# Optimization experiments

Hardware: AMD Instinct MI355X
Metric: run time of the kernel (lower is better)

The kernel has to match this reference:

```python
import jax, jax.numpy as jnp
import numpy as np

B, T, S, A = 4, 10, 6, 6
HID, L, IMG = 512, 6, 128
NCH = 16  # spatial-softmax channels
_px, _py = np.meshgrid(np.linspace(-1.0, 1.0, IMG), np.linspace(-1.0, 1.0, IMG))
POSX = jnp.asarray(_px.reshape(-1), jnp.float32)
POSY = jnp.asarray(_py.reshape(-1), jnp.float32)


def _conv_relu(x, w, b):
    y = jax.lax.conv_general_dilated(x, w, (1, 1), 'SAME',
                                     dimension_numbers=('NCHW', 'OIHW', 'NCHW'))
    return jax.nn.relu(y + b[None, :, None, None])


def _cnn_ss(x, ws, bs):
    for w, b in zip(ws, bs):
        x = _conv_relu(x, w, b)
    n = x.shape[0]
    attn = jax.nn.softmax(x.reshape(n, NCH, -1), axis=-1)  # (n, 16, H*W)
    ex = attn @ POSX  # (n, 16)
    ey = attn @ POSY
    return jnp.stack([ex, ey], axis=-1).reshape(n, 2 * NCH)  # (n, 32)


def _lstm_cell(x, h, c, wih, whh, bih, bhh):
    g = x @ wih.T + bih + h @ whh.T + bhh
    i, f, gg, o = jnp.split(g, 4, axis=-1)  # torch LSTMCell gate order i,f,g,o
    c2 = jax.nn.sigmoid(f) * c + jax.nn.sigmoid(i) * jnp.tanh(gg)
    h2 = jax.nn.sigmoid(o) * jnp.tanh(c2)
    return h2, c2


def setup_inputs() -> dict:
    key = jax.random.key(0)
    ks = iter(jax.random.split(key, 64))

    def nrm(shape, s=0.05):
        return jax.random.normal(next(ks), shape, dtype=jnp.float32) * s

    inp = {
        'seq_img_main': nrm((B, T, 3, IMG, IMG), 1.0),
        'seq_img_secondary': nrm((B, T, 3, IMG, IMG), 1.0),
        'seq_states': nrm((B, T, S), 1.0),
    }
    chans = [(32, 3), (64, 32), (128, 64), (16, 128)]
    for cam in ('m', 's'):
        for j, (o, ci) in enumerate(chans):
            inp[f'{cam}_w{j}'] = nrm((o, ci, 3, 3))
            inp[f'{cam}_b{j}'] = nrm((o,))
    in0, inr = S + 64, HID + 64  # 70 and 576
    inp['wih0'] = nrm((4 * HID, in0)); inp['whh0'] = nrm((4 * HID, HID))
    inp['bih0'] = nrm((4 * HID,)); inp['bhh0'] = nrm((4 * HID,))
    inp['wih_r'] = nrm((L - 1, 4 * HID, inr)); inp['whh_r'] = nrm((L - 1, 4 * HID, HID))
    inp['bih_r'] = nrm((L - 1, 4 * HID)); inp['bhh_r'] = nrm((L - 1, 4 * HID))
    inp['out_w'] = nrm((A, inr)); inp['out_b'] = nrm((A,))
    return inp


def reference(seq_img_main, seq_img_secondary, seq_states,
              m_w0, m_b0, m_w1, m_b1, m_w2, m_b2, m_w3, m_b3,
              s_w0, s_b0, s_w1, s_b1, s_w2, s_b2, s_w3, s_b3,
              wih0, whh0, bih0, bhh0, wih_r, whh_r, bih_r, bhh_r,
              out_w, out_b):
    b, t = seq_img_main.shape[:2]
    fm = _cnn_ss(seq_img_main.reshape(b * t, 3, IMG, IMG),
                 [m_w0, m_w1, m_w2, m_w3], [m_b0, m_b1, m_b2, m_b3])
    fs = _cnn_ss(seq_img_secondary.reshape(b * t, 3, IMG, IMG),
                 [s_w0, s_w1, s_w2, s_w3], [s_b0, s_b1, s_b2, s_b3])
    img = jnp.concatenate([fm, fs], axis=-1).reshape(b, t, 64)  # (B,T,64)

    h0 = jnp.zeros((L, b, HID), jnp.float32)
    c0 = jnp.zeros((L, b, HID), jnp.float32)

    def step(carry, xt):
        h, c = carry
        st, im = xt  # (B,S), (B,64)
        x = jnp.concatenate([st, im], axis=-1)
        hn, cn = _lstm_cell(x, h[0], c[0], wih0, whh0, bih0, bhh0)
        hs, cs = [hn], [cn]
        for l in range(L - 1):
            x = jnp.concatenate([hs[-1], im], axis=-1)
            hl, cl = _lstm_cell(x, h[l + 1], c[l + 1],
                                wih_r[l], whh_r[l], bih_r[l], bhh_r[l])
            hs.append(hl); cs.append(cl)
        out = jnp.concatenate([hs[-1], im], axis=-1) @ out_w.T + out_b
        return (jnp.stack(hs), jnp.stack(cs)), out

    _, outs = jax.lax.scan(step, (h0, c0),
                           (seq_states.transpose(1, 0, 2), img.transpose(1, 0, 2)))
    return outs.transpose(1, 0, 2)  # (B,T,A)
```

## Files before the change

### kernel.cpp

```cpp
#include <hip/hip_runtime.h>
#include <hip/hip_bf16.h>
#include <math.h>

typedef __hip_bfloat16 bf16;
typedef short bf16x8 __attribute__((ext_vector_type(8)));
typedef float f32x4 __attribute__((ext_vector_type(4)));

static constexpr int HWPX = 16384;
static constexpr int NBL  = 16;

__device__ inline float sigmoidf_(float x) { return 1.0f / (1.0f + expf(-x)); }
__device__ inline float bflo(unsigned u) { return __uint_as_float(u << 16); }
__device__ inline float bfhi(unsigned u) { return __uint_as_float(u & 0xffff0000u); }
__device__ inline int swz(int x) { return (x ^ (x >> 2)) & 3; }

__device__ inline void gll16(const bf16* g, short* l) {
    __builtin_amdgcn_global_load_lds(
        (const __attribute__((address_space(1))) void*)g,
        (__attribute__((address_space(3))) void*)l, 16, 0, 0);
}

__device__ inline int flag_ld(const int* p) {
    return __hip_atomic_load(p, __ATOMIC_RELAXED, __HIP_MEMORY_SCOPE_AGENT);
}
__device__ inline void flag_st(int* p, int v) {
    __hip_atomic_store(p, v, __ATOMIC_RELAXED, __HIP_MEMORY_SCOPE_AGENT);
}
__device__ inline unsigned long long devload2(const float* p) {
    return __hip_atomic_load((const unsigned long long*)p,
                             __ATOMIC_RELAXED, __HIP_MEMORY_SCOPE_AGENT);
}
__device__ inline void devstore(float* p, float v) {
    __hip_atomic_store(p, v, __ATOMIC_RELAXED, __HIP_MEMORY_SCOPE_AGENT);
}

__global__ __launch_bounds__(256) void prep_lstm_k(
    const float* __restrict__ wih0, const float* __restrict__ whh0,
    const float* __restrict__ wihr, const float* __restrict__ whhr,
    bf16* __restrict__ d0, bf16* __restrict__ d1,
    bf16* __restrict__ d2, bf16* __restrict__ d3)
{
    const size_t nA = 2048ull * 72, nB = 2048ull * 512;
    const size_t nC = 5ull * 2048 * 576, nD = 5ull * 2048 * 512;
    for (size_t i = blockIdx.x * 256ull + threadIdx.x; i < nA + nB + nC + nD;
         i += (size_t)gridDim.x * 256) {
        if (i < nA) {
            int c = (int)(i % 72), r = (int)(i / 72);
            d0[i] = __float2bfloat16(c < 70 ? wih0[(size_t)r * 70 + c] : 0.f);
        } else if (i < nA + nB) {
            size_t k = i - nA; d1[k] = __float2bfloat16(whh0[k]);
        } else if (i < nA + nB + nC) {
            size_t k = i - nA - nB; d2[k] = __float2bfloat16(wihr[k]);
        } else {
            size_t k = i - nA - nB - nC; d3[k] = __float2bfloat16(whhr[k]);
        }
    }
}

struct ConvW {
    const float* src[8];
    bf16* dst[8];
};

__global__ __launch_bounds__(256) void prep_conv_k(ConvW a)
{
    const int sizes[4] = {3072, 18432, 73728, 18432};
    const int cins[4] = {3, 32, 64, 128};
    const int couts[4] = {32, 64, 128, 16};
    int total = 2 * 113664;
    for (int idx = blockIdx.x * 256 + threadIdx.x; idx < total; idx += gridDim.x * 256) {
        int i = idx, cam = 0;
        if (i >= 113664) { cam = 1; i -= 113664; }
        int layer = 0;
        while (layer < 3 && i >= sizes[layer]) { i -= sizes[layer]; ++layer; }
        const float* w = a.src[cam * 4 + layer];
        bf16* d = a.dst[cam * 4 + layer];
        if (layer == 0) {
            int k = i & 31, co = (i >> 5) & 31, ky = i >> 10;
            int kx = k >> 3, c = k & 7;
            float v = (kx < 3 && c < 3) ? w[((co * 3 + c) * 3 + ky) * 3 + kx] : 0.f;
            d[i] = __float2bfloat16(v);
        } else {
            int CIN = cins[layer], COUT = couts[layer], KC = CIN / 32;
            int e = i & 7;
            int t2 = i >> 3;
            int co = t2 % COUT;
            int t3 = t2 / COUT;
            int q = t3 & 3;
            int t4 = t3 >> 2;
            int kc = t4 % KC;
            int tap = t4 / KC;
            d[i] = __float2bfloat16(w[((size_t)(co * CIN + kc * 32 + q * 8 + e)) * 9 + tap]);
        }
    }
}

__global__ __launch_bounds__(256) void conv0_nhwc(
    const float* __restrict__ srcm, const float* __restrict__ srcs,
    const bf16* __restrict__ w0m, const bf16* __restrict__ w0s,
    const float* __restrict__ bm, const float* __restrict__ bs,
    bf16* __restrict__ out, int c0)
{
    const int y = blockIdx.x;
    const int cam = blockIdx.y;
    const int img = blockIdx.z;
    const int ci_ = cam * gridDim.z + img;
    const float* inImg = (cam ? srcs : srcm) + (size_t)(c0 + img) * 3 * HWPX;
    const bf16* wT0 = cam ? w0s : w0m;
    const float* bias = cam ? bs : bm;
    const int tid = threadIdx.x;
    const int wave = tid >> 6, lane = tid & 63;
    const int wm = wave & 1, wn = wave >> 1;
    const int q = lane >> 4, n16 = lane & 15;

    __shared__ short smem[3 * 130 * 16];

    for (int d = tid; d < 3 * 130; d += 256) {
        int x = d % 130, r = d / 130;
        int yy = y + r - 1, xx = x - 1;
        bf16 v8[8];
#pragma unroll
        for (int c = 0; c < 8; ++c) v8[c] = __float2bfloat16(0.f);
        if ((unsigned)yy < 128u && (unsigned)xx < 128u) {
            int o = yy * 128 + xx;
            v8[0] = __float2bfloat16(inImg[o]);
            v8[1] = __float2bfloat16(inImg[HWPX + o]);
            v8[2] = __float2bfloat16(inImg[2 * HWPX + o]);
        }
        *(bf16x8*)(void*)&smem[(r * 130 + x) * 16] = *(bf16x8*)(void*)v8;
        *(bf16x8*)(void*)&smem[(r * 130 + x) * 16 + 8] = (bf16x8)0;
    }
    __syncthreads();

    f32x4 acc[4];
#pragma unroll
    for (int nt = 0; nt < 4; ++nt) acc[nt] = f32x4{0.f, 0.f, 0.f, 0.f};

    const int co = wm * 16 + n16;
#pragma unroll
    for (int ky = 0; ky < 3; ++ky) {
        bf16x8 aF = *(const bf16x8*)(const void*)(wT0 + ((size_t)(ky * 32 + co) * 32) + q * 8);
#pragma unroll
        for (int nt = 0; nt < 4; ++nt) {
            int x = (wn * 4 + nt) * 16 + n16;
            int off = (q < 3) ? (ky * 130 + x + q) * 16 : (ky * 130 + x) * 16 + 8;
            bf16x8 bF = *(const bf16x8*)(const void*)&smem[off];
            acc[nt] = __builtin_amdgcn_mfma_f32_16x16x32_bf16(aF, bF, acc[nt], 0, 0, 0);
        }
    }

    int co0 = wm * 16 + q * 4;
#pragma unroll
    for (int nt = 0; nt < 4; ++nt) {
        int x = (wn * 4 + nt) * 16 + n16;
        bf16 tmp[4];
#pragma unroll
        for (int r = 0; r < 4; ++r) {
            float v = acc[nt][r] + bias[co0 + r];
            tmp[r] = __float2bfloat16(v > 0.f ? v : 0.f);
        }
        *reinterpret_cast<uint2*>(out + ((size_t)ci_ * HWPX + y * 128 + x) * 32 + co0)
            = *reinterpret_cast<uint2*>(tmp);
    }
}

template <int CIN, int COUT>
__global__ __launch_bounds__(256, 4) void conv2r(
    const bf16* __restrict__ in, const bf16* __restrict__ wTm,
    const bf16* __restrict__ wTs, const float* __restrict__ bm,
    const float* __restrict__ bs, bf16* __restrict__ out,
    const char* __restrict__ zpage)
{
    constexpr int KC = CIN / 32;
    constexpr int NB = (KC > 1) ? 2 : 1;
    constexpr int MW = COUT / 32;
    constexpr int SLOTS = 4 * 264;

    const int y0 = (blockIdx.x >> 1) * 2;
    const int x0 = (blockIdx.x & 1) * 64;
    const int cam = blockIdx.y;
    const int img = blockIdx.z;
    const int ci_ = cam * gridDim.z + img;
    const bf16* wT = cam ? wTs : wTm;
    const float* bias = cam ? bs : bm;
    const int tid = threadIdx.x;
    const int wave = tid >> 6, lane = tid & 63;
    const int wrow = wave >> 1, wm = wave & 1;
    const int q = lane >> 4, n16 = lane & 15;

    __shared__ short smem[NB][SLOTS * 8];
    const bf16* inImg = in + (size_t)ci_ * HWPX * CIN;

    const bf16* sptr[5];
#pragma unroll
    for (int it = 0; it < 5; ++it) {
        int s = it * 256 + tid;
        int r = s / 264, s2 = s - r * 264;
        int sx = s2 >> 2;
        int g = (s2 & 3) ^ swz(sx);
        int yy = y0 + r - 1, xx = x0 + sx - 1;
        bool ok = (s < SLOTS) && ((unsigned)yy < 128u) && ((unsigned)xx < 128u);
        sptr[it] = ok ? inImg + ((size_t)yy * 128 + xx) * CIN + g * 8
                      : (const bf16*)(zpage + (tid & 255) * 16);
    }
    auto stage = [&](int kc, int buf) {
#pragma unroll
        for (int it = 0; it < 5; ++it) {
            if (it * 256 + tid < SLOTS)
                gll16(sptr[it] + kc * 32, &smem[buf][it * 2048 + wave * 512]);
        }
    };

    f32x4 acc[MW][4];
#pragma unroll
    for (int mt = 0; mt < MW; ++mt)
#pragma unroll
        for (int nt = 0; nt < 4; ++nt) acc[mt][nt] = f32x4{0.f, 0.f, 0.f, 0.f};

    stage(0, 0);
    for (int kc = 0; kc < KC; ++kc) {
        __syncthreads();
        if (kc + 1 < KC) stage(kc + 1, (kc + 1) % NB);
        const short* sb = smem[kc % NB];
#pragma unroll
        for (int ky = 0; ky < 3; ++ky) {
#pragma unroll
            for (int kx = 0; kx < 3; ++kx) {
                bf16x8 aF[MW];
#pragma unroll
                for (int mt = 0; mt < MW; ++mt) {
                    int co = (wm * MW + mt) * 16 + n16;
                    aF[mt] = *(const bf16x8*)(const void*)(wT +
                        ((((size_t)(ky * 3 + kx) * KC + kc) * 4 + q) * COUT + co) * 8);
                }
#pragma unroll
                for (int nt = 0; nt < 4; ++nt) {
                    int xt = nt * 16 + n16 + kx;
                    int slot = (wrow + ky) * 264 + xt * 4 + (q ^ swz(xt));
                    bf16x8 bF = *(const bf16x8*)(const void*)&sb[slot * 8];
#pragma unroll
                    for (int mt = 0; mt < MW; ++mt)
                        acc[mt][nt] = __builtin_amdgcn_mfma_f32_16x16x32_bf16(
                            aF[mt], bF, acc[mt][nt], 0, 0, 0);
                }
            }
        }
    }

    const int y = y0 + wrow;
#pragma unroll
    for (int mt = 0; mt < MW; ++mt) {
        int co0 = (wm * MW + mt) * 16 + q * 4;
#pragma unroll
        for (int nt = 0; nt < 4; ++nt) {
            int x = x0 + nt * 16 + n16;
            bf16 tmp[4];
#pragma unroll
            for (int r = 0; r < 4; ++r) {
                float v = acc[mt][nt][r] + bias[co0 + r];
                tmp[r] = __float2bfloat16(v > 0.f ? v : 0.f);
            }
            *reinterpret_cast<uint2*>(out + ((size_t)ci_ * HWPX + y * 128 + x) * COUT + co0)
                = *reinterpret_cast<uint2*>(tmp);
        }
    }
}

__global__ __launch_bounds__(256, 6) void conv4_xs(
    const bf16* __restrict__ in, const bf16* __restrict__ wTm,
    const bf16* __restrict__ wTs, const float* __restrict__ bm,
    const float* __restrict__ bs,
    float* __restrict__ partial,
    const char* __restrict__ zpage, int c0)
{
    constexpr int CIN = 128, COUT = 16, KC = 4;
    constexpr int SLOTS = 3 * 66 * 4;
    const int y = blockIdx.x >> 1;
    const int xh = blockIdx.x & 1;
    const int x0 = xh * 64;
    const int cam = blockIdx.y;
    const int img = blockIdx.z;
    const int ci_ = cam * gridDim.z + img;
    const int gimg = cam * 40 + c0 + img;
    const bf16* wT = cam ? wTs : wTm;
    const float* bias = cam ? bs : bm;
    const int tid = threadIdx.x;
    const int wave = tid >> 6, lane = tid & 63;
    const int q = lane >> 4, n16 = lane & 15;

    __shared__ short smem[2][SLOTS * 8];
    __shared__ float sred[3][4][16];
    const bf16* inImg = in + (size_t)ci_ * HWPX * CIN;

    const bf16* sptr[4];
#pragma unroll
    for (int it = 0; it < 4; ++it) {
        int s = it * 256 + tid;
        int r = s / 264, s2 = s - r * 264;
        int sx = s2 >> 2;
        int g = (s2 & 3) ^ swz(sx);
        int yy = y + r - 1, xx = x0 + sx - 1;
        bool ok = (s < SLOTS) && ((unsigned)yy < 128u) && ((unsigned)xx < 128u);
        sptr[it] = ok ? inImg + ((size_t)yy * 128 + xx) * CIN + g * 8
                      : (const bf16*)(zpage + (tid & 255) * 16);
    }
    auto stage = [&](int kc, int buf) {
#pragma unroll
        for (int it = 0; it < 4; ++it) {
            if (it * 256 + tid < SLOTS)
                gll16(sptr[it] + kc * 32, &smem[buf][it * 2048 + wave * 512]);
        }
    };

    f32x4 acc = f32x4{0.f, 0.f, 0.f, 0.f};

    stage(0, 0);
    for (int kc = 0; kc < KC; ++kc) {
        __syncthreads();
        if (kc + 1 < KC) stage(kc + 1, (kc + 1) & 1);
        const short* sb = smem[kc & 1];
#pragma unroll
        for (int ky = 0; ky < 3; ++ky) {
#pragma unroll
            for (int kx = 0; kx < 3; ++kx) {
                bf16x8 aF = *(const bf16x8*)(const void*)(wT +
                    ((((size_t)(ky * 3 + kx) * KC + kc) * 4 + q) * COUT + n16) * 8);
                int xt = wave * 16 + n16 + kx;
                int slot = xt * 4 + (q ^ swz(xt));
                bf16x8 bF = *(const bf16x8*)(const void*)&sb[ky * 2112 + slot * 8];
                acc = __builtin_amdgcn_mfma_f32_16x16x32_bf16(aF, bF, acc, 0, 0, 0);
            }
        }
    }

    float v[4];
    int x = x0 + wave * 16 + n16;
    float px = -1.f + (2.f / 127.f) * x;
#pragma unroll
    for (int r = 0; r < 4; ++r) {
        float t = acc[r] + bias[q * 4 + r];
        v[r] = t > 0.f ? t : 0.f;
    }
    float M[4];
#pragma unroll
    for (int r = 0; r < 4; ++r) {
        M[r] = v[r];
        M[r] = fmaxf(M[r], __shfl_xor(M[r], 1));
        M[r] = fmaxf(M[r], __shfl_xor(M[r], 2));
        M[r] = fmaxf(M[r], __shfl_xor(M[r], 4));
        M[r] = fmaxf(M[r], __shfl_xor(M[r], 8));
    }
    if (n16 == 0)
#pragma unroll
        for (int r = 0; r < 4; ++r) sred[0][wave][q * 4 + r] = M[r];
    __syncthreads();
#pragma unroll
    for (int r = 0; r < 4; ++r) {
        M[r] = fmaxf(fmaxf(sred[0][0][q * 4 + r], sred[0][1][q * 4 + r]),
                     fmaxf(sred[0][2][q * 4 + r], sred[0][3][q * 4 + r]));
    }
    float s[4], sx[4];
#pragma unroll
    for (int r = 0; r < 4; ++r) {
        float e = expf(v[r] - M[r]);
        s[r] = e; sx[r] = e * px;
        s[r] += __shfl_xor(s[r], 1);  sx[r] += __shfl_xor(sx[r], 1);
        s[r] += __shfl_xor(s[r], 2);  sx[r] += __shfl_xor(sx[r], 2);
        s[r] += __shfl_xor(s[r], 4);  sx[r] += __shfl_xor(sx[r], 4);
        s[r] += __shfl_xor(s[r], 8);  sx[r] += __shfl_xor(sx[r], 8);
    }
    __syncthreads();
    if (n16 == 0)
#pragma unroll
        for (int r = 0; r < 4; ++r) {
            sred[1][wave][q * 4 + r] = s[r];
            sred[2][wave][q * 4 + r] = sx[r];
        }
    __syncthreads();
    if (tid < 16) {
        float S = sred[1][0][tid] + sred[1][1][tid] + sred[1][2][tid] + sred[1][3][tid];
        float SX = sred[2][0][tid] + sred[2][1][tid] + sred[2][2][tid] + sred[2][3][tid];
        float Mv = fmaxf(fmaxf(sred[0][0][tid], sred[0][1][tid]),
                         fmaxf(sred[0][2][tid], sred[0][3][tid]));
        float* pp = partial + (((size_t)gimg * 16 + tid) * 256 + (y * 2 + xh)) * 4;
        pp[0] = Mv; pp[1] = S; pp[2] = SX;
    }
}

__global__ __launch_bounds__(256) void ssmerge_k(
    const float* __restrict__ partial, float* __restrict__ featm,
    float* __restrict__ feats)
{
    const int img = blockIdx.x;
    const int cam = img / 40, li = img % 40;
    float* feat = cam ? feats : featm;
    const int tid = threadIdx.x;
    const int co = tid >> 4, s = tid & 15;
    const float* base = partial + ((size_t)img * 16 + co) * 256 * 4;
    float M = -1e30f, S = 0.f, SX = 0.f, SY = 0.f;
    for (int i = s; i < 256; i += 16) {
        float m = base[i * 4], sv = base[i * 4 + 1], sxv = base[i * 4 + 2];
        float py = -1.f + (2.f / 127.f) * (i >> 1);
        float Mn = fmaxf(M, m);
        float w0 = expf(M - Mn), w1 = expf(m - Mn);
        S = S * w0 + sv * w1;
        SX = SX * w0 + sxv * w1;
        SY = SY * w0 + sv * py * w1;
        M = Mn;
    }
#pragma unroll
    for (int mask = 1; mask < 16; mask <<= 1) {
        float Mo = __shfl_xor(M, mask), So = __shfl_xor(S, mask);
        float SXo = __shfl_xor(SX, mask), SYo = __shfl_xor(SY, mask);
        float Mn = fmaxf(M, Mo);
        float w0 = expf(M - Mn), w1 = expf(Mo - Mn);
        S = S * w0 + So * w1; SX = SX * w0 + SXo * w1; SY = SY * w0 + SYo * w1;
        M = Mn;
    }
    if (s == 0) {
        feat[(size_t)li * 32 + 2 * co] = SX / S;
        feat[(size_t)li * 32 + 2 * co + 1] = SY / S;
    }
}

__device__ inline float imgfeat(const float* featm, const float* feats,
                                int b, int t, int k)
{
    int idx = (b * 10 + t) * 32;
    return k < 32 ? featm[idx + k] : feats[idx + k - 32];
}

template <int NB1>
__device__ inline void cell_mm(const bf16* __restrict__ wih,
                               const bf16* __restrict__ whh,
                               const float* __restrict__ xs0,
                               int j, int sub, float (&dg)[4][4])
{
    constexpr int K1 = NB1 * 8;
    constexpr int XS = K1 + 512;
#pragma unroll
    for (int r = 0; r < 4; ++r) {
        const uint4* __restrict__ w1 =
            reinterpret_cast<const uint4*>(wih + (size_t)(j + r * 512) * K1);
#pragma unroll
        for (int g0 = 0; g0 < NB1; g0 += 8) {
            int g = g0 + sub;
            if (g0 + 7 < NB1 || g < NB1) {
                uint4 u = w1[g];
                float a0 = bflo(u.x), a1 = bfhi(u.x), a2 = bflo(u.y), a3 = bfhi(u.y);
                float a4 = bflo(u.z), a5 = bfhi(u.z), a6 = bflo(u.w), a7 = bfhi(u.w);
#pragma unroll
                for (int b = 0; b < 4; ++b) {
                    const float* xp = xs0 + b * XS + g * 8;
                    dg[r][b] += a0 * xp[0] + a1 * xp[1] + a2 * xp[2] + a3 * xp[3]
                              + a4 * xp[4] + a5 * xp[5] + a6 * xp[6] + a7 * xp[7];
                }
            }
        }
        const uint4* __restrict__ w2 =
            reinterpret_cast<const uint4*>(whh + (size_t)(j + r * 512) * 512);
#pragma unroll
        for (int gi = 0; gi < 8; ++gi) {
            int g = gi * 8 + sub;
            uint4 u = w2[g];
            float a0 = bflo(u.x), a1 = bfhi(u.x), a2 = bflo(u.y), a3 = bfhi(u.y);
            float a4 = bflo(u.z), a5 = bfhi(u.z), a6 = bflo(u.w), a7 = bfhi(u.w);
#pragma unroll
            for (int b = 0; b < 4; ++b) {
                const float* xp = xs0 + b * XS + K1 + g * 8;
                dg[r][b] += a0 * xp[0] + a1 * xp[1] + a2 * xp[2] + a3 * xp[3]
                          + a4 * xp[4] + a5 * xp[5] + a6 * xp[6] + a7 * xp[7];
            }
        }
    }
}

template <int NB1>
__device__ inline void lstm_layer_loop(
    int l, int bx,
    const bf16* __restrict__ wih, const bf16* __restrict__ whh,
    const float* __restrict__ bih, const float* __restrict__ bhh,
    const float* __restrict__ states,
    const float* __restrict__ featm, const float* __restrict__ feats,
    float* __restrict__ hAll, float* __restrict__ cst,
    int* __restrict__ fl, float* __restrict__ xs)
{
    constexpr int K1 = NB1 * 8;
    constexpr int XS = K1 + 512;
    const int tid = threadIdx.x;
    const int jloc = tid >> 3;
    const int sub = tid & 7;
    const int j = bx * 32 + jloc;

    for (int t = 0; t < 10; ++t) {
        if (l > 0 && tid < 16) {
            while (flag_ld(&fl[(l - 1) * 16 + tid]) < t + 1)
                __builtin_amdgcn_s_sleep(1);
        }
        if (t > 0 && tid >= 64 && tid < 80) {
            while (flag_ld(&fl[l * 16 + (tid - 64)]) < t)
                __builtin_amdgcn_s_sleep(1);
        }
        __syncthreads();

        const float* hprev = (l == 0) ? nullptr
                           : hAll + ((size_t)(t + 1) * 6 + (l - 1)) * 2048;
        const float* hold  = hAll + ((size_t)t * 6 + l) * 2048;
        float* hnew        = hAll + ((size_t)(t + 1) * 6 + l) * 2048;

        if (NB1 == 72) {
            for (int i = tid; i < 4 * 512; i += 256) {
                int bb = i >> 9, kk = i & 511;
                union { unsigned long long u; float f[2]; } cv;
                int base;
                if (kk < 256) { cv.u = devload2(&hprev[bb * 512 + kk * 2]); base = bb * XS + kk * 2; }
                else { cv.u = devload2(&hold[bb * 512 + (kk - 256) * 2]); base = bb * XS + 576 + (kk - 256) * 2; }
                xs[base] = cv.f[0]; xs[base + 1] = cv.f[1];
            }
            {
                int bb = tid >> 6, k = tid & 63;
                xs[bb * XS + 512 + k] = imgfeat(featm, feats, bb, t, k);
            }
        } else {
            for (int i = tid; i < 4 * 256; i += 256) {
                int bb = i >> 8, kk = i & 255;
                union { unsigned long long u; float f[2]; } cv;
                cv.u = devload2(&hold[bb * 512 + kk * 2]);
                int base = bb * XS + 72 + kk * 2;
                xs[base] = cv.f[0]; xs[base + 1] = cv.f[1];
            }
            for (int i = tid; i < 4 * 72; i += 256) {
                int bb = i / 72, k = i - bb * 72;
                float v = (k < 6) ? states[(bb * 10 + t) * 6 + k]
                                  : (k < 70 ? imgfeat(featm, feats, bb, t, k - 6) : 0.f);
                xs[bb * XS + k] = v;
            }
        }
        __syncthreads();

        float dg[4][4] = {{0.f, 0.f, 0.f, 0.f}, {0.f, 0.f, 0.f, 0.f},
                          {0.f, 0.f, 0.f, 0.f}, {0.f, 0.f, 0.f, 0.f}};
        cell_mm<NB1>(wih, whh, xs, j, sub, dg);

#pragma unroll
        for (int r = 0; r < 4; ++r)
#pragma unroll
            for (int b = 0; b < 4; ++b) {
                dg[r][b] += __shfl_xor(dg[r][b], 1);
                dg[r][b] += __shfl_xor(dg[r][b], 2);
                dg[r][b] += __shfl_xor(dg[r][b], 4);
            }

        if (sub == 0) {
            float b0 = bih[j] + bhh[j];
            float b1 = bih[j + 512] + bhh[j + 512];
            float b2 = bih[j + 1024] + bhh[j + 1024];
            float b3 = bih[j + 1536] + bhh[j + 1536];
#pragma unroll
            for (int b = 0; b < 4; ++b) {
                float gi = dg[0][b] + b0;
                float gf = dg[1][b] + b1;
                float gg = dg[2][b] + b2;
                float go = dg[3][b] + b3;
                float cp = cst[b * 512 + j];
                float c2 = sigmoidf_(gf) * cp + sigmoidf_(gi) * tanhf(gg);
                float h2 = sigmoidf_(go) * tanhf(c2);
                cst[b * 512 + j] = c2;
                devstore(&hnew[b * 512 + j], h2);
            }
        }
        __syncthreads();
        if (tid == 0) flag_st(&fl[l * 16 + bx], t + 1);
    }
}

__global__ __launch_bounds__(256) void lstm_pipe_k(
    const bf16* __restrict__ wih0p, const bf16* __restrict__ whh0b,
    const bf16* __restrict__ wihrb, const bf16* __restrict__ whhrb,
    const float* __restrict__ bih0, const float* __restrict__ bhh0,
    const float* __restrict__ bihr, const float* __restrict__ bhhr,
    const float* __restrict__ states,
    const float* __restrict__ featm, const float* __restrict__ feats,
    float* __restrict__ hAll, float* __restrict__ cAll,
    const float* __restrict__ out_w, const float* __restrict__ out_b,
    float* __restrict__ out, int* __restrict__ fl)
{
    const int gb = blockIdx.x;
    const int tid = threadIdx.x;
    __shared__ float xs[4 * 1088];

    if (gb == 6 * NBL) {
        for (int t = 0; t < 10; ++t) {
            if (tid < 16) {
                while (flag_ld(&fl[5 * 16 + tid]) < t + 1)
                    __builtin_amdgcn_s_sleep(1);
            }
            __syncthreads();
            const float* h5 = hAll + ((size_t)(t + 1) * 6 + 5) * 2048;
            int p = tid >> 3, sub = tid & 7;
            if (p < 24) {
                int b = p / 6, a = p % 6;
                const float* wr = out_w + a * 576;
                float acc = 0.f;
                for (int k = sub; k < 256; k += 8) {
                    union { unsigned long long u; float f[2]; } cv;
                    cv.u = devload2(&h5[b * 512 + k * 2]);
                    acc += wr[k * 2] * cv.f[0] + wr[k * 2 + 1] * cv.f[1];
                }
                for (int k = sub; k < 64; k += 8)
                    acc += wr[512 + k] * imgfeat(featm, feats, b, t, k);
                acc += __shfl_xor(acc, 1);
                acc += __shfl_xor(acc, 2);
                acc += __shfl_xor(acc, 4);
                if (sub == 0) out[(b * 10 + t) * 6 + a] = acc + out_b[a];
            }
            __syncthreads();
        }
        return;
    }

    const int l = gb / NBL;
    const int bx = gb % NBL;

    const bf16 *wih, *whh;
    const float *bih, *bhh;
    if (l == 0) { wih = wih0p; whh = whh0b; bih = bih0; bhh = bhh0; }
    else {
        wih = wihrb + (size_t)(l - 1) * 2048 * 576;
        whh = whhrb + (size_t)(l - 1) * 2048 * 512;
        bih = bihr + (l - 1) * 2048;
        bhh = bhhr + (l - 1) * 2048;
    }
    float* cst = cAll + (size_t)l * 2048;

    if (l > 0) {
        const int jloc = tid >> 3, sub = tid & 7;
        const int j = bx * 32 + jloc;
        unsigned wsum = 0;
        for (int r = 0; r < 4; ++r) {
            const uint4* w1 = reinterpret_cast<const uint4*>(wih + (size_t)(j + r * 512) * 576);
            for (int g = sub; g < 72; g += 8) { uint4 u = w1[g]; wsum ^= u.x ^ u.w; }
            const uint4* w2 = reinterpret_cast<const uint4*>(whh + (size_t)(j + r * 512) * 512);
            for (int g = sub; g < 64; g += 8) { uint4 u = w2[g]; wsum ^= u.x ^ u.w; }
        }
        asm volatile("" :: "v"(wsum));
    }

    if (l == 0)
        lstm_layer_loop<9>(l, bx, wih, whh, bih, bhh, states, featm, feats,
                           hAll, cst, fl, xs);
    else
        lstm_layer_loop<72>(l, bx, wih, whh, bih, bhh, states, featm, feats,
                            hAll, cst, fl, xs);
}

extern "C" void kernel_launch(void* const* d_in, const int* in_sizes, int n_in,
                              void* d_out, int out_size, void* d_ws, size_t ws_size,
                              hipStream_t stream)
{
    const float* seq_m = (const float*)d_in[0];
    const float* seq_s = (const float*)d_in[1];
    const float* states = (const float*)d_in[2];
    const float *cw[2][4], *cb[2][4];
    for (int cam = 0; cam < 2; ++cam)
        for (int j = 0; j < 4; ++j) {
            cw[cam][j] = (const float*)d_in[3 + cam * 8 + j * 2];
            cb[cam][j] = (const float*)d_in[3 + cam * 8 + j * 2 + 1];
        }
    const float* wih0  = (const float*)d_in[19];
    const float* whh0  = (const float*)d_in[20];
    const float* bih0  = (const float*)d_in[21];
    const float* bhh0  = (const float*)d_in[22];
    const float* wih_r = (const float*)d_in[23];
    const float* whh_r = (const float*)d_in[24];
    const float* bih_r = (const float*)d_in[25];
    const float* bhh_r = (const float*)d_in[26];
    const float* out_w = (const float*)d_in[27];
    const float* out_b = (const float*)d_in[28];
    float* out = (float*)d_out;

    char* wsc = (char*)d_ws;
    auto carve = [&](size_t bytes) {
        char* p = wsc;
        wsc += (bytes + 255) & ~(size_t)255;
        return p;
    };
    float* featm = (float*)carve(40 * 32 * 4);
    float* feats = (float*)carve(40 * 32 * 4);
    float* hAll  = (float*)carve((size_t)11 * 6 * 2048 * 4);
    float* cAll  = (float*)carve((size_t)6 * 2048 * 4);
    char*  zpage = carve(8192);
    int*   lcnt  = (int*)carve((size_t)6 * NBL * 4);
    float* partial = (float*)carve((size_t)80 * 16 * 256 * 4 * 4);
    const int wtElts[4] = {3072, 18432, 73728, 18432};
    bf16* wT[2][4];
    for (int cam = 0; cam < 2; ++cam)
        for (int j = 0; j < 4; ++j) wT[cam][j] = (bf16*)carve(wtElts[j] * 2);
    bf16* wih0p = (bf16*)carve((size_t)2048 * 72 * 2);
    bf16* whh0b = (bf16*)carve((size_t)2048 * 512 * 2);
    bf16* wihrb = (bf16*)carve((size_t)5 * 2048 * 576 * 2);
    bf16* whhrb = (bf16*)carve((size_t)5 * 2048 * 512 * 2);

    size_t used = (size_t)(wsc - (char*)d_ws);
    size_t rem = ws_size > used ? ws_size - used : 0;
    int CHI = 1;
    const int cands[7] = {20, 10, 8, 5, 4, 2, 1};
    for (int i = 0; i < 7; ++i) {
        size_t need = (size_t)2 * cands[i] * (128 + 64) * HWPX * 2;
        if (need <= rem) { CHI = cands[i]; break; }
    }
    bf16* bufA = (bf16*)carve((size_t)2 * CHI * HWPX * 128 * 2);
    bf16* bufB = (bf16*)carve((size_t)2 * CHI * HWPX * 64 * 2);

    hipMemsetAsync(hAll, 0, 6 * 2048 * 4, stream);
    hipMemsetAsync(cAll, 0, 6 * 2048 * 4, stream);
    hipMemsetAsync(zpage, 0, 8192, stream);
    hipMemsetAsync(lcnt, 0, 6 * NBL * 4, stream);

    prep_lstm_k<<<2048, 256, 0, stream>>>(wih0, whh0, wih_r, whh_r,
                                          wih0p, whh0b, wihrb, whhrb);
    ConvW cwArg;
    for (int cam = 0; cam < 2; ++cam)
        for (int j = 0; j < 4; ++j) {
            cwArg.src[cam * 4 + j] = cw[cam][j];
            cwArg.dst[cam * 4 + j] = wT[cam][j];
        }
    prep_conv_k<<<888, 256, 0, stream>>>(cwArg);

    for (int c0 = 0; c0 < 40; c0 += CHI) {
        int ch = (40 - c0) < CHI ? (40 - c0) : CHI;
        conv0_nhwc<<<dim3(128, 2, ch), 256, 0, stream>>>(
            seq_m, seq_s, wT[0][0], wT[1][0], cb[0][0], cb[1][0], bufA, c0);
        conv2r<32, 64><<<dim3(128, 2, ch), 256, 0, stream>>>(
            bufA, wT[0][1], wT[1][1], cb[0][1], cb[1][1], bufB, zpage);
        conv2r<64, 128><<<dim3(128, 2, ch), 256, 0, stream>>>(
            bufB, wT[0][2], wT[1][2], cb[0][2], cb[1][2], bufA, zpage);
        conv4_xs<<<dim3(256, 2, ch), 256, 0, stream>>>(
            bufA, wT[0][3], wT[1][3], cb[0][3], cb[1][3], partial, zpage, c0);
    }
    ssmerge_k<<<80, 256, 0, stream>>>(partial, featm, feats);

    lstm_pipe_k<<<dim3(6 * NBL + 1), 256, 0, stream>>>(
        wih0p, whh0b, wihrb, whhrb, bih0, bhh0, bih_r, bhh_r,
        states, featm, feats, hAll, cAll, out_w, out_b, out, lcnt);
}
```

Before: 1.238 ms.

## Replace flag-synchronized persistent LSTM pipeline with per-diagonal kernel launches

Removes the persistent LSTM kernel, which used global atomic flags and spin-waits to chain layers and timesteps. The LSTM is now run as 16 wavefront-diagonal launches, each computing every (layer, t) cell with l+t=d plus the output projection, so kernel boundaries supply the ordering. This drops the spin-wait polling, the atomic loads and stores, and the weight-prefetch warmup. In exchange it adds 16 launch overheads, and weights are refetched on every launch with no persistence across steps.

```diff
diff --git a/kernel.cpp b/kernel.cpp
--- a/kernel.cpp
+++ b/kernel.cpp
@@ -18,20 +18,6 @@
     __builtin_amdgcn_global_load_lds(
         (const __attribute__((address_space(1))) void*)g,
         (__attribute__((address_space(3))) void*)l, 16, 0, 0);
-}
-
-__device__ inline int flag_ld(const int* p) {
-    return __hip_atomic_load(p, __ATOMIC_RELAXED, __HIP_MEMORY_SCOPE_AGENT);
-}
-__device__ inline void flag_st(int* p, int v) {
-    __hip_atomic_store(p, v, __ATOMIC_RELAXED, __HIP_MEMORY_SCOPE_AGENT);
-}
-__device__ inline unsigned long long devload2(const float* p) {
-    return __hip_atomic_load((const unsigned long long*)p,
-                             __ATOMIC_RELAXED, __HIP_MEMORY_SCOPE_AGENT);
-}
-__device__ inline void devstore(float* p, float v) {
-    __hip_atomic_store(p, v, __ATOMIC_RELAXED, __HIP_MEMORY_SCOPE_AGENT);
 }
 
 __global__ __launch_bounds__(256) void prep_lstm_k(
@@ -476,14 +462,14 @@
 }
 
 template <int NB1>
-__device__ inline void lstm_layer_loop(
-    int l, int bx,
+__device__ inline void cell_step(
+    int l, int t, int bx,
     const bf16* __restrict__ wih, const bf16* __restrict__ whh,
     const float* __restrict__ bih, const float* __restrict__ bhh,
     const float* __restrict__ states,
     const float* __restrict__ featm, const float* __restrict__ feats,
     float* __restrict__ hAll, float* __restrict__ cst,
-    int* __restrict__ fl, float* __restrict__ xs)
+    float* __restrict__ xs)
 {
     constexpr int K1 = NB1 * 8;
     constexpr int XS = K1 + 512;
@@ -492,89 +478,79 @@
     const int sub = tid & 7;
     const int j = bx * 32 + jloc;
 
-    for (int t = 0; t < 10; ++t) {
-        if (l > 0 && tid < 16) {
-            while (flag_ld(&fl[(l - 1) * 16 + tid]) < t + 1)
-                __builtin_amdgcn_s_sleep(1);
-        }
-        if (t > 0 && tid >= 64 && tid < 80) {
-            while (flag_ld(&fl[l * 16 + (tid - 64)]) < t)
-                __builtin_amdgcn_s_sleep(1);
-        }
-        __syncthreads();
-
-        const float* hprev = (l == 0) ? nullptr
-                           : hAll + ((size_t)(t + 1) * 6 + (l - 1)) * 2048;
-        const float* hold  = hAll + ((size_t)t * 6 + l) * 2048;
-        float* hnew        = hAll + ((size_t)(t + 1) * 6 + l) * 2048;
-
-        if (NB1 == 72) {
-            for (int i = tid; i < 4 * 512; i += 256) {
-                int bb = i >> 9, kk = i & 511;
-                union { unsigned long long u; float f[2]; } cv;
-                int base;
-                if (kk < 256) { cv.u = devload2(&hprev[bb * 512 + kk * 2]); base = bb * XS + kk * 2; }
-                else { cv.u = devload2(&hold[bb * 512 + (kk - 256) * 2]); base = bb * XS + 576 + (kk - 256) * 2; }
-                xs[base] = cv.f[0]; xs[base + 1] = cv.f[1];
+    const float* hprev = (l == 0) ? nullptr
+                       : hAll + ((size_t)(t + 1) * 6 + (l - 1)) * 2048;
+    const float* hold  = hAll + ((size_t)t * 6 + l) * 2048;
+    float* hnew        = hAll + ((size_t)(t + 1) * 6 + l) * 2048;
+
+    if (NB1 == 72) {
+        for (int i = tid; i < 4 * 512; i += 256) {
+            int bb = i >> 9, kk = i & 511;
+            float2 cv;
+            int base;
+            if (kk < 256) {
+                cv = *reinterpret_cast<const float2*>(&hprev[bb * 512 + kk * 2]);
+                base = bb * XS + kk * 2;
+            } else {
+                cv = *reinterpret_cast<const float2*>(&hold[bb * 512 + (kk - 256) * 2]);
+                base = bb * XS + 576 + (kk - 256) * 2;
             }
-            {
-                int bb = tid >> 6, k = tid & 63;
-                xs[bb * XS + 512 + k] = imgfeat(featm, feats, bb, t, k);
-            }
-        } else {
-            for (int i = tid; i < 4 * 256; i += 256) {
-                int bb = i >> 8, kk = i & 255;
-                union { unsigned long long u; float f[2]; } cv;
-                cv.u = devload2(&hold[bb * 512 + kk * 2]);
-                int base = bb * XS + 72 + kk * 2;
-                xs[base] = cv.f[0]; xs[base + 1] = cv.f[1];
-            }
-            for (int i = tid; i < 4 * 72; i += 256) {
-                int bb = i / 72, k = i - bb * 72;
-                float v = (k < 6) ? states[(bb * 10 + t) * 6 + k]
-                                  : (k < 70 ? imgfeat(featm, feats, bb, t, k - 6) : 0.f);
-                xs[bb * XS + k] = v;
-            }
-        }
-        __syncthreads();
-
-        float dg[4][4] = {{0.f, 0.f, 0.f, 0.f}, {0.f, 0.f, 0.f, 0.f},
-                          {0.f, 0.f, 0.f, 0.f}, {0.f, 0.f, 0.f, 0.f}};
-        cell_mm<NB1>(wih, whh, xs, j, sub, dg);
-
-#pragma unroll
-        for (int r = 0; r < 4; ++r)
-#pragma unroll
-            for (int b = 0; b < 4; ++b) {
-                dg[r][b] += __shfl_xor(dg[r][b], 1);
-                dg[r][b] += __shfl_xor(dg[r][b], 2);
-                dg[r][b] += __shfl_xor(dg[r][b], 4);
-            }
-
-        if (sub == 0) {
-            float b0 = bih[j] + bhh[j];
-            float b1 = bih[j + 512] + bhh[j + 512];
-            float b2 = bih[j + 1024] + bhh[j + 1024];
-            float b3 = bih[j + 1536] + bhh[j + 1536];
-#pragma unroll
-            for (int b = 0; b < 4; ++b) {
-                float gi = dg[0][b] + b0;
-                float gf = dg[1][b] + b1;
-                float gg = dg[2][b] + b2;
-                float go = dg[3][b] + b3;
-                float cp = cst[b * 512 + j];
-                float c2 = sigmoidf_(gf) * cp + sigmoidf_(gi) * tanhf(gg);
-                float h2 = sigmoidf_(go) * tanhf(c2);
-                cst[b * 512 + j] = c2;
-                devstore(&hnew[b * 512 + j], h2);
-            }
-        }
-        __syncthreads();
-        if (tid == 0) flag_st(&fl[l * 16 + bx], t + 1);
-    }
-}
-
-__global__ __launch_bounds__(256) void lstm_pipe_k(
+            xs[base] = cv.x; xs[base + 1] = cv.y;
+        }
+        {
+            int bb = tid >> 6, k = tid & 63;
+            xs[bb * XS + 512 + k] = imgfeat(featm, feats, bb, t, k);
+        }
+    } else {
+        for (int i = tid; i < 4 * 256; i += 256) {
+            int bb = i >> 8, kk = i & 255;
+            float2 cv = *reinterpret_cast<const float2*>(&hold[bb * 512 + kk * 2]);
+            int base = bb * XS + 72 + kk * 2;
+            xs[base] = cv.x; xs[base + 1] = cv.y;
+        }
+        for (int i = tid; i < 4 * 72; i += 256) {
+            int bb = i / 72, k = i - bb * 72;
+            float v = (k < 6) ? states[(bb * 10 + t) * 6 + k]
+                              : (k < 70 ? imgfeat(featm, feats, bb, t, k - 6) : 0.f);
+            xs[bb * XS + k] = v;
+        }
+    }
+    __syncthreads();
+
+    float dg[4][4] = {{0.f, 0.f, 0.f, 0.f}, {0.f, 0.f, 0.f, 0.f},
+                      {0.f, 0.f, 0.f, 0.f}, {0.f, 0.f, 0.f, 0.f}};
+    cell_mm<NB1>(wih, whh, xs, j, sub, dg);
+
+#pragma unroll
+    for (int r = 0; r < 4; ++r)
+#pragma unroll
+        for (int b = 0; b < 4; ++b) {
+            dg[r][b] += __shfl_xor(dg[r][b], 1);
+            dg[r][b] += __shfl_xor(dg[r][b], 2);
+            dg[r][b] += __shfl_xor(dg[r][b], 4);
+        }
+
+    if (sub == 0) {
+        float b0 = bih[j] + bhh[j];
+        float b1 = bih[j + 512] + bhh[j + 512];
+        float b2 = bih[j + 1024] + bhh[j + 1024];
+        float b3 = bih[j + 1536] + bhh[j + 1536];
+#pragma unroll
+        for (int b = 0; b < 4; ++b) {
+            float gi = dg[0][b] + b0;
+            float gf = dg[1][b] + b1;
+            float gg = dg[2][b] + b2;
+            float go = dg[3][b] + b3;
+            float cp = cst[b * 512 + j];
+            float c2 = sigmoidf_(gf) * cp + sigmoidf_(gi) * tanhf(gg);
+            float h2 = sigmoidf_(go) * tanhf(c2);
+            cst[b * 512 + j] = c2;
+            hnew[b * 512 + j] = h2;
+        }
+    }
+}
+
+__global__ __launch_bounds__(256) void lstm_diag2_k(
     const bf16* __restrict__ wih0p, const bf16* __restrict__ whh0b,
     const bf16* __restrict__ wihrb, const bf16* __restrict__ whhrb,
     const float* __restrict__ bih0, const float* __restrict__ bhh0,
@@ -583,75 +559,50 @@
     const float* __restrict__ featm, const float* __restrict__ feats,
     float* __restrict__ hAll, float* __restrict__ cAll,
     const float* __restrict__ out_w, const float* __restrict__ out_b,
-    float* __restrict__ out, int* __restrict__ fl)
-{
-    const int gb = blockIdx.x;
+    float* __restrict__ out, int d)
+{
+    const int l = blockIdx.y;
+    const int bx = blockIdx.x;
     const int tid = threadIdx.x;
     __shared__ float xs[4 * 1088];
 
-    if (gb == 6 * NBL) {
-        for (int t = 0; t < 10; ++t) {
-            if (tid < 16) {
-                while (flag_ld(&fl[5 * 16 + tid]) < t + 1)
-                    __builtin_amdgcn_s_sleep(1);
-            }
-            __syncthreads();
-            const float* h5 = hAll + ((size_t)(t + 1) * 6 + 5) * 2048;
-            int p = tid >> 3, sub = tid & 7;
-            if (p < 24) {
-                int b = p / 6, a = p % 6;
-                const float* wr = out_w + a * 576;
-                float acc = 0.f;
-                for (int k = sub; k < 256; k += 8) {
-                    union { unsigned long long u; float f[2]; } cv;
-                    cv.u = devload2(&h5[b * 512 + k * 2]);
-                    acc += wr[k * 2] * cv.f[0] + wr[k * 2 + 1] * cv.f[1];
-                }
-                for (int k = sub; k < 64; k += 8)
-                    acc += wr[512 + k] * imgfeat(featm, feats, b, t, k);
-                acc += __shfl_xor(acc, 1);
-                acc += __shfl_xor(acc, 2);
-                acc += __shfl_xor(acc, 4);
-                if (sub == 0) out[(b * 10 + t) * 6 + a] = acc + out_b[a];
-            }
-            __syncthreads();
-        }
+    if (l == 6) {
+        int t = d - 6;
+        if (t < 0 || t >= 10 || bx != 0) return;
+        const float* h5 = hAll + ((size_t)(t + 1) * 6 + 5) * 2048;
+        int p = tid >> 3, sub = tid & 7;
+        if (p >= 24) return;
+        int b = p / 6, a = p % 6;
+        const float* wr = out_w + a * 576;
+        float acc = 0.f;
+        for (int k = sub; k < 256; k += 8) {
+            float2 cv = *reinterpret_cast<const float2*>(&h5[b * 512 + k * 2]);
+            acc += wr[k * 2] * cv.x + wr[k * 2 + 1] * cv.y;
+        }
+        for (int k = sub; k < 64; k += 8)
+            acc += wr[512 + k] * imgfeat(featm, feats, b, t, k);
+        acc += __shfl_xor(acc, 1);
+        acc += __shfl_xor(acc, 2);
+        acc += __shfl_xor(acc, 4);
+        if (sub == 0) out[(b * 10 + t) * 6 + a] = acc + out_b[a];
         return;
     }
 
-    const int l = gb / NBL;
-    const int bx = gb % NBL;
-
-    const bf16 *wih, *whh;
-    const float *bih, *bhh;
-    if (l == 0) { wih = wih0p; whh = whh0b; bih = bih0; bhh = bhh0; }
-    else {
-        wih = wihrb + (size_t)(l - 1) * 2048 * 576;
-        whh = whhrb + (size_t)(l - 1) * 2048 * 512;
-        bih = bihr + (l - 1) * 2048;
-        bhh = bhhr + (l - 1) * 2048;
-    }
+    const int t = d - l;
+    if (t < 0 || t >= 10) return;
+
     float* cst = cAll + (size_t)l * 2048;
-
-    if (l > 0) {
-        const int jloc = tid >> 3, sub = tid & 7;
-        const int j = bx * 32 + jloc;
-        unsigned wsum = 0;
-        for (int r = 0; r < 4; ++r) {
-            const uint4* w1 = reinterpret_cast<const uint4*>(wih + (size_t)(j + r * 512) * 576);
-            for (int g = sub; g < 72; g += 8) { uint4 u = w1[g]; wsum ^= u.x ^ u.w; }
-            const uint4* w2 = reinterpret_cast<const uint4*>(whh + (size_t)(j + r * 512) * 512);
-            for (int g = sub; g < 64; g += 8) { uint4 u = w2[g]; wsum ^= u.x ^ u.w; }
-        }
-        asm volatile("" :: "v"(wsum));
-    }
-
-    if (l == 0)
-        lstm_layer_loop<9>(l, bx, wih, whh, bih, bhh, states, featm, feats,
-                           hAll, cst, fl, xs);
-    else
-        lstm_layer_loop<72>(l, bx, wih, whh, bih, bhh, states, featm, feats,
-                            hAll, cst, fl, xs);
+    if (l == 0) {
+        cell_step<9>(0, t, bx, wih0p, whh0b, bih0, bhh0,
+                     states, featm, feats, hAll, cst, xs);
+    } else {
+        const bf16* wih = wihrb + (size_t)(l - 1) * 2048 * 576;
+        const bf16* whh = whhrb + (size_t)(l - 1) * 2048 * 512;
+        const float* bih = bihr + (l - 1) * 2048;
+        const float* bhh = bhhr + (l - 1) * 2048;
+        cell_step<72>(l, t, bx, wih, whh, bih, bhh,
+                      states, featm, feats, hAll, cst, xs);
+    }
 }
 
 extern "C" void kernel_launch(void* const* d_in, const int* in_sizes, int n_in,
@@ -690,7 +641,6 @@
     float* hAll  = (float*)carve((size_t)11 * 6 * 2048 * 4);
     float* cAll  = (float*)carve((size_t)6 * 2048 * 4);
     char*  zpage = carve(8192);
-    int*   lcnt  = (int*)carve((size_t)6 * NBL * 4);
     float* partial = (float*)carve((size_t)80 * 16 * 256 * 4 * 4);
     const int wtElts[4] = {3072, 18432, 73728, 18432};
     bf16* wT[2][4];
@@ -715,7 +665,6 @@
     hipMemsetAsync(hAll, 0, 6 * 2048 * 4, stream);
     hipMemsetAsync(cAll, 0, 6 * 2048 * 4, stream);
     hipMemsetAsync(zpage, 0, 8192, stream);
-    hipMemsetAsync(lcnt, 0, 6 * NBL * 4, stream);
 
     prep_lstm_k<<<2048, 256, 0, stream>>>(wih0, whh0, wih_r, whh_r,
                                           wih0p, whh0b, wihrb, whhrb);
@@ -740,7 +689,9 @@
     }
     ssmerge_k<<<80, 256, 0, stream>>>(partial, featm, feats);
 
-    lstm_pipe_k<<<dim3(6 * NBL + 1), 256, 0, stream>>>(
-        wih0p, whh0b, wihrb, whhrb, bih0, bhh0, bih_r, bhh_r,
-        states, featm, feats, hAll, cAll, out_w, out_b, out, lcnt);
-}
+    for (int d = 0; d < 16; ++d) {
+        lstm_diag2_k<<<dim3(16, 7), 256, 0, stream>>>(
+            wih0p, whh0b, wihrb, whhrb, bih0, bhh0, bih_r, bhh_r,
+            states, featm, feats, hAll, cAll, out_w, out_b, out, d);
+    }
+}
```

After: 1.149 ms. -7.2%, faster.
